# Optimization experiments

Measured on AMD Instinct MI355X. Metric: run time of the kernel, lower is better.

## Reference

```python
import jax, jax.numpy as jnp
import numpy as np
from functools import partial

# Module hyperparameters (from init_kwargs)
T, C_IN, H, W_DIM = 128, 16, 64, 64
C_OUT, KH, KW = 64, 3, 3
PAD = ((1, 1), (1, 1))  # (top,bottom),(left,right) -> symmetric here
STRIDES = (1, 1)
F_V_THRESH = 8.0
F_V_THRESH_LOW = -1.0
F_V_RESET = 0.0
# fVSubtract is None -> reset-to-value branch


def setup_inputs() -> dict:
    key = jax.random.key(0)
    kx, kw, kb = jax.random.split(key, 3)
    x = jax.random.uniform(kx, (T, C_IN, H, W_DIM), dtype=jnp.float32)
    fan_in = C_IN * KH * KW
    bound = 1.0 / np.sqrt(fan_in)
    W = jax.random.uniform(kw, (C_OUT, C_IN, KH, KW), dtype=jnp.float32,
                           minval=-bound, maxval=bound)
    b = jax.random.uniform(kb, (C_OUT,), dtype=jnp.float32,
                           minval=-bound, maxval=bound)
    return {"x": x, "W": W, "b": b}


def _spiking_conv(x, W, b):
    # conv over all timesteps at once (time is the conv batch dim): [T, C_out, H, W]
    conv_out = jax.lax.conv_general_dilated(
        x, W, window_strides=STRIDES, padding=PAD,
        dimension_numbers=("NCHW", "OIHW", "NCHW"))
    conv_out = conv_out + b[None, :, None, None]

    def step(state, conv_t):
        state = state + conv_t
        spikes = (state >= F_V_THRESH).astype(conv_t.dtype)
        # reset-to-value branch (fVSubtract is None)
        state = spikes * F_V_RESET + state * (1.0 - spikes)
        # nn.Threshold(v, v): x if x > v else v
        state = jnp.where(state > F_V_THRESH_LOW, state, F_V_THRESH_LOW)
        return state, spikes

    init_state = jnp.zeros(conv_out.shape[1:], dtype=conv_out.dtype)
    _, num_spikes = jax.lax.scan(step, init_state, conv_out)
    return num_spikes  # [T, C_out, H, W] float (0/1)


def reference(x, W, b):
    return _spiking_conv(x, W, b)
```

## Files before the change

### kernel.cpp

```cpp
#include <hip/hip_runtime.h>

#define T_STEPS 128
#define CIN     16
#define HH      64
#define WW      64
#define COUT    64
#define HWSZ    (HH * WW)
#define CHW     (COUT * HWSZ)
#define XCHW    (CIN * HWSZ)

#define TILE    32
#define HALO    34
#define LSTR    36
#define PLANE   (HALO * LSTR)
#define NST     (CIN * HALO * HALO)
#define WBLK    40

__global__ void transpose_w(const float* __restrict__ W, float* __restrict__ Wtr) {
    int e = blockIdx.x * 256 + threadIdx.x;
    if (e >= COUT * CIN * 9) return;
    int co = e / (CIN * 9);
    int r  = e - co * (CIN * 9);
    int ci = r / 9;
    int k  = r - ci * 9;
    Wtr[((co >> 2) * CIN + ci) * WBLK + (co & 3) * 9 + k] = W[e];
}

__global__ __launch_bounds__(512, 4)
void spiking_conv_pass1(const float* __restrict__ x, const float* __restrict__ Wtr,
                        const float* __restrict__ b, float* __restrict__ out) {
    __shared__ float xs[CIN * PLANE];

    const int tid  = threadIdx.x;
    const int t    = 127 - blockIdx.y;
    const int coh  = blockIdx.x & 1;
    const int tile = blockIdx.x >> 1;
    const int h0   = (tile >> 1) * TILE;
    const int w0   = (tile & 1) * TILE;

    const float* xt = x + t * XCHW;
    {
        float vbuf[19]; int ibuf[19];
#pragma unroll
        for (int k = 0; k < 18; ++k) {
            unsigned e = tid + k * 512;
            unsigned ci = e / (HALO * HALO);
            unsigned rem = e - ci * (HALO * HALO);
            unsigned r  = rem / HALO;
            unsigned c  = rem - r * HALO;
            int gh = h0 - 1 + (int)r;
            int gw = w0 - 1 + (int)c;
            bool inb = (unsigned)gh < HH && (unsigned)gw < WW;
            vbuf[k] = inb ? xt[ci * HWSZ + gh * WW + gw] : 0.f;
            ibuf[k] = ci * PLANE + r * LSTR + c;
        }
#pragma unroll
        for (int k = 0; k < 18; ++k) xs[ibuf[k]] = vbuf[k];
#pragma unroll
        for (int k = 0; k < 19; ++k) {
            unsigned e = tid + (18 + k) * 512;
            unsigned ci = e / (HALO * HALO);
            unsigned rem = e - ci * (HALO * HALO);
            unsigned r  = rem / HALO;
            unsigned c  = rem - r * HALO;
            int gh = h0 - 1 + (int)r;
            int gw = w0 - 1 + (int)c;
            bool inb = e < NST && (unsigned)gh < HH && (unsigned)gw < WW;
            vbuf[k] = inb ? xt[ci * HWSZ + gh * WW + gw] : 0.f;
            ibuf[k] = (e < NST) ? (int)(ci * PLANE + r * LSTR + c) : -1;
        }
#pragma unroll
        for (int k = 0; k < 19; ++k)
            if (ibuf[k] >= 0) xs[ibuf[k]] = vbuf[k];
    }
    __syncthreads();

    const int cog = __builtin_amdgcn_readfirstlane(tid >> 8);
    const int sp  = tid & 255;
    const int pr0 = sp >> 3;
    const int pc0 = (sp & 7) * 4;
    float* outt = out + t * CHW;

    float acc[16][4];
#pragma unroll
    for (int j = 0; j < 16; ++j)
#pragma unroll
        for (int p = 0; p < 4; ++p) acc[j][p] = 0.f;

#pragma unroll 1
    for (int ci = 0; ci < CIN; ++ci) {
        float xv[3][6];
#pragma unroll
        for (int dr = 0; dr < 3; ++dr) {
            const float* row = &xs[ci * PLANE + (pr0 + dr) * LSTR + pc0];
            float4 a  = *(const float4*)row;
            float2 c2 = *(const float2*)(row + 4);
            xv[dr][0] = a.x;  xv[dr][1] = a.y;
            xv[dr][2] = a.z;  xv[dr][3] = a.w;
            xv[dr][4] = c2.x; xv[dr][5] = c2.y;
        }
#pragma unroll
        for (int g = 0; g < 4; ++g) {
            const int g4 = coh * 8 + cog * 4 + g;
            const float* wb = Wtr + (g4 * CIN + ci) * WBLK;
            float w[36];
#pragma unroll
            for (int i = 0; i < 36; ++i) w[i] = wb[i];
#pragma unroll
            for (int jj = 0; jj < 4; ++jj)
#pragma unroll
                for (int ky = 0; ky < 3; ++ky)
#pragma unroll
                    for (int kx = 0; kx < 3; ++kx) {
                        const float wv = w[jj * 9 + ky * 3 + kx];
#pragma unroll
                        for (int p = 0; p < 4; ++p)
                            acc[g * 4 + jj][p] += wv * xv[ky][kx + p];
                    }
        }
    }

#pragma unroll
    for (int g = 0; g < 4; ++g)
#pragma unroll
        for (int jj = 0; jj < 4; ++jj) {
            const int co = coh * 32 + cog * 16 + g * 4 + jj;
            const float bias = b[co];
            float4 o;
            o.x = acc[g * 4 + jj][0] + bias;
            o.y = acc[g * 4 + jj][1] + bias;
            o.z = acc[g * 4 + jj][2] + bias;
            o.w = acc[g * 4 + jj][3] + bias;
            *(float4*)&outt[co * HWSZ + (h0 + pr0) * WW + (w0 + pc0)] = o;
        }
}

#define SCH 256
#define TCK 32

__global__ __launch_bounds__(256)
void spiking_scan_chunk(float* __restrict__ io, float* __restrict__ state,
                        int t0) {
    __shared__ float tile[TCK][SCH];
    const int tid  = threadIdx.x;
    const int wv   = tid >> 6;
    const int ln   = tid & 63;
    const int base = blockIdx.x * SCH;

#pragma unroll
    for (int i = 0; i < 8; ++i) {
        const int r = wv * 8 + i;
        const float* g = io + (size_t)(t0 + r) * CHW + base;
        __builtin_amdgcn_global_load_lds(
            (const __attribute__((address_space(1))) void*)(g + ln * 4),
            (__attribute__((address_space(3))) void*)&tile[r][0], 16, 0, 0);
    }
    __syncthreads();

    float s = 0.f;
    if (t0 != 0) s = state[base + tid];
#pragma unroll
    for (int r = 0; r < TCK; ++r) {
        float v = tile[r][tid];
        s += v;
        const bool sp = (s >= 8.0f);
        tile[r][tid] = sp ? 1.0f : 0.0f;
        s = sp ? 0.0f : s;
        s = fmaxf(s, -1.0f);
    }
    state[base + tid] = s;
    __syncthreads();

#pragma unroll
    for (int i = 0; i < 8; ++i) {
        const int r = wv * 8 + i;
        float4 v = *(const float4*)&tile[r][ln * 4];
        *(float4*)(io + (size_t)(t0 + r) * CHW + base + ln * 4) = v;
    }
}

extern "C" void kernel_launch(void* const* d_in, const int* in_sizes, int n_in,
                              void* d_out, int out_size, void* d_ws, size_t ws_size,
                              hipStream_t stream) {
    const float* x = (const float*)d_in[0];
    const float* W = (const float*)d_in[1];
    const float* b = (const float*)d_in[2];
    float* out = (float*)d_out;
    float* Wtr   = (float*)d_ws;
    float* state = (float*)((char*)d_ws + 65536);

    transpose_w<<<36, 256, 0, stream>>>(W, Wtr);

    dim3 g1(8, 128);
    spiking_conv_pass1<<<g1, 512, 0, stream>>>(x, Wtr, b, out);

    for (int c = 0; c < T_STEPS / TCK; ++c)
        spiking_scan_chunk<<<CHW / SCH, 256, 0, stream>>>(out, state, c * TCK);
}
```

Before: 275.8 us.

## Write conv output time-transposed to workspace and scan in one kernel

The conv kernel can now write its output into a workspace in a layout where the 128 timesteps of each row segment are adjacent, grouped by (channel,row). A single scan kernel then walks time per element with one thread per element and writes spikes straight to the output. This replaces the four chunked scan launches and their in-place read-modify-write of the output buffer with one launch and one pass. The cost is a 128 MB workspace, and the path is only used when the workspace is large enough; otherwise the old path runs.

New measurement: 281.1 us. About the same (+1.9%).

```diff
diff --git a/kernel.cpp b/kernel.cpp
--- a/kernel.cpp
+++ b/kernel.cpp
@@ -16,6 +16,9 @@
 #define NST     (CIN * HALO * HALO)
 #define WBLK    40
 
+#define WS_WTR_BYTES   65536
+#define WS_TPOSE_BYTES ((size_t)WS_WTR_BYTES + (size_t)CHW * T_STEPS * 4)
+
 __global__ void transpose_w(const float* __restrict__ W, float* __restrict__ Wtr) {
     int e = blockIdx.x * 256 + threadIdx.x;
     if (e >= COUT * CIN * 9) return;
@@ -26,9 +29,10 @@
     Wtr[((co >> 2) * CIN + ci) * WBLK + (co & 3) * 9 + k] = W[e];
 }
 
+template <bool TPOSE>
 __global__ __launch_bounds__(512, 4)
 void spiking_conv_pass1(const float* __restrict__ x, const float* __restrict__ Wtr,
-                        const float* __restrict__ b, float* __restrict__ out) {
+                        const float* __restrict__ b, float* __restrict__ dst) {
     __shared__ float xs[CIN * PLANE];
 
     const int tid  = threadIdx.x;
@@ -79,7 +83,6 @@
     const int sp  = tid & 255;
     const int pr0 = sp >> 3;
     const int pc0 = (sp & 7) * 4;
-    float* outt = out + t * CHW;
 
     float acc[16][4];
 #pragma unroll
@@ -131,8 +134,39 @@
             o.y = acc[g * 4 + jj][1] + bias;
             o.z = acc[g * 4 + jj][2] + bias;
             o.w = acc[g * 4 + jj][3] + bias;
-            *(float4*)&outt[co * HWSZ + (h0 + pr0) * WW + (w0 + pc0)] = o;
-        }
+            if (TPOSE) {
+                const int E = co * 64 + (h0 + pr0);
+                *(float4*)&dst[(size_t)(E * 128 + t) * 64 + (w0 + pc0)] = o;
+            } else {
+                *(float4*)&dst[(size_t)t * CHW + co * HWSZ +
+                               (h0 + pr0) * WW + (w0 + pc0)] = o;
+            }
+        }
+}
+
+__global__ __launch_bounds__(256)
+void spiking_scan_tpose(const float* __restrict__ ws, float* __restrict__ out) {
+    const int tid = threadIdx.x;
+    const int ec  = tid >> 6;
+    const int i   = tid & 63;
+    const int E   = blockIdx.x * 4 + ec;
+    const int eb  = E * 64 + i;
+    const float* col = ws + (size_t)E * (T_STEPS * 64) + i;
+    float s = 0.f;
+#pragma unroll 1
+    for (int tb = 0; tb < T_STEPS / 8; ++tb) {
+        float v[8];
+#pragma unroll
+        for (int k = 0; k < 8; ++k) v[k] = col[(tb * 8 + k) * 64];
+#pragma unroll
+        for (int k = 0; k < 8; ++k) {
+            s += v[k];
+            const bool spk = (s >= 8.0f);
+            out[(size_t)(tb * 8 + k) * CHW + eb] = spk ? 1.0f : 0.0f;
+            s = spk ? 0.0f : s;
+            s = fmaxf(s, -1.0f);
+        }
+    }
 }
 
 #define SCH 256
@@ -163,9 +197,9 @@
     for (int r = 0; r < TCK; ++r) {
         float v = tile[r][tid];
         s += v;
-        const bool sp = (s >= 8.0f);
-        tile[r][tid] = sp ? 1.0f : 0.0f;
-        s = sp ? 0.0f : s;
+        const bool spk = (s >= 8.0f);
+        tile[r][tid] = spk ? 1.0f : 0.0f;
+        s = spk ? 0.0f : s;
         s = fmaxf(s, -1.0f);
     }
     state[base + tid] = s;
@@ -186,14 +220,20 @@
     const float* W = (const float*)d_in[1];
     const float* b = (const float*)d_in[2];
     float* out = (float*)d_out;
-    float* Wtr   = (float*)d_ws;
-    float* state = (float*)((char*)d_ws + 65536);
+    float* Wtr = (float*)d_ws;
 
     transpose_w<<<36, 256, 0, stream>>>(W, Wtr);
 
     dim3 g1(8, 128);
-    spiking_conv_pass1<<<g1, 512, 0, stream>>>(x, Wtr, b, out);
-
-    for (int c = 0; c < T_STEPS / TCK; ++c)
-        spiking_scan_chunk<<<CHW / SCH, 256, 0, stream>>>(out, state, c * TCK);
-}
+
+    if (ws_size >= WS_TPOSE_BYTES) {
+        float* cws = (float*)((char*)d_ws + WS_WTR_BYTES);
+        spiking_conv_pass1<true><<<g1, 512, 0, stream>>>(x, Wtr, b, cws);
+        spiking_scan_tpose<<<CHW / 256, 256, 0, stream>>>(cws, out);
+    } else {
+        float* state = (float*)((char*)d_ws + WS_WTR_BYTES);
+        spiking_conv_pass1<false><<<g1, 512, 0, stream>>>(x, Wtr, b, out);
+        for (int c = 0; c < T_STEPS / TCK; ++c)
+            spiking_scan_chunk<<<CHW / SCH, 256, 0, stream>>>(out, state, c * TCK);
+    }
+}
```
